# Kernel tuning notes

Measured on AMD Instinct MI355X. Metric: run time of the kernel, lower is better.

Reference implementation:

```python
import jax, jax.numpy as jnp
import numpy as np

N_VARS = 28
HID = 64
BATCH = 32768
BN_EPS = 1e-5


def _lin_init(key, fan_in, shape):
    bound = 1.0 / np.sqrt(fan_in)
    return jax.random.uniform(key, shape, minval=-bound, maxval=bound, dtype=jnp.float32)


def setup_inputs() -> dict:
    key = jax.random.key(0)
    ks = jax.random.split(key, 8)
    n, h = N_VARS, HID
    X = jax.random.normal(ks[0], (BATCH, n), dtype=jnp.float32)
    W_logits = jax.random.uniform(ks[1], (n, n), minval=-0.01, maxval=0.01, dtype=jnp.float32)
    # per-mechanism (grouped) weights, stacked on leading mechanism axis n
    W1 = _lin_init(ks[2], n, (n, h, n)); b1 = _lin_init(ks[3], n, (n, h))
    W2 = _lin_init(ks[4], h, (n, h, h)); b2 = _lin_init(ks[5], h, (n, h))
    W3 = _lin_init(ks[6], h, (n, 1, h)); b3 = _lin_init(ks[7], h, (n, 1))
    gamma1 = jnp.ones((n, h)); beta1 = jnp.zeros((n, h))
    gamma2 = jnp.ones((n, h)); beta2 = jnp.zeros((n, h))
    return {"X": X, "W_logits": W_logits,
            "W1": W1, "b1": b1, "gamma1": gamma1, "beta1": beta1,
            "W2": W2, "b2": b2, "gamma2": gamma2, "beta2": beta2,
            "W3": W3, "b3": b3}


def _bn(x, gamma, beta):
    # x: [n, B, h]; batch stats over B (training-mode BatchNorm1d, biased var)
    m = x.mean(axis=1, keepdims=True)
    v = ((x - m) ** 2).mean(axis=1, keepdims=True)
    return gamma[:, None, :] * (x - m) * jax.lax.rsqrt(v + BN_EPS) + beta[:, None, :]


def reference(X, W_logits, W1, b1, gamma1, beta1, W2, b2, gamma2, beta2, W3, b3):
    n = W_logits.shape[0]
    # adjacency: sigmoid with zeroed diagonal
    W = jax.nn.sigmoid(W_logits) * (1.0 - jnp.eye(n, dtype=W_logits.dtype))
    # fuse the parent mask into the first layer's weights: one grouped GEMM
    # instead of n_vars separate masked matmuls
    W1_eff = W1 * W[:, None, :]                               # [n, h, n]
    h1 = jnp.einsum('bd,nhd->nbh', X, W1_eff) + b1[:, None, :]  # [n, B, h]
    a1 = jax.nn.gelu(_bn(h1, gamma1, beta1), approximate=False)
    h2 = jnp.einsum('nbh,ngh->nbg', a1, W2) + b2[:, None, :]
    a2 = jax.nn.gelu(_bn(h2, gamma2, beta2), approximate=False)
    out = jnp.einsum('nbh,noh->nbo', a2, W3) + b3[:, None, :]   # [n, B, 1]
    X_hat = out[:, :, 0].T                                     # [B, n]
    return (X_hat, W)
```

## Files before the change

### kernel.cpp

```cpp
#include <hip/hip_runtime.h>
#include <hip/hip_bf16.h>
#include <math.h>

typedef float  f4 __attribute__((ext_vector_type(4)));
typedef short  s8 __attribute__((ext_vector_type(8)));
typedef short  s4 __attribute__((ext_vector_type(4)));
typedef int    i2 __attribute__((ext_vector_type(2)));

#define NV 28
#define NB 32768
#define BN_EPS 1e-5f
#define NSLOT 434

#define SUM2_OFF   0
#define SSQ2_OFF   1792
#define BIAS1_OFF  3584
#define GATE_OFF   5376
#define PART_OFF   9472
#define BF_BASE_F  120640
#define W2B_OFF_S  57344
#define XBF_OFF_S  172032
#define H2_BYTE_OFF 2924544ull
#define H2_BYTES    117440512ull

#define SMEM_BYTES 34816
#define GMAIN 896

__device__ __forceinline__ float gelu_f(float x) {
    float x2 = x * x;
    float z  = x * __builtin_fmaf(x2, -0.10294324f, -2.3022082f);
    float t  = __builtin_amdgcn_exp2f(z);
    return x * __builtin_amdgcn_rcpf(1.0f + t);
}
__device__ __forceinline__ unsigned short f2bf(float x) {
    unsigned u = __builtin_bit_cast(unsigned, x);
    return (unsigned short)((u + 0x7fffu + ((u >> 16) & 1u)) >> 16);
}
__device__ __forceinline__ int bfpack(float a, float b) {
    unsigned ua = __builtin_bit_cast(unsigned, a) + 0x8000u;
    unsigned ub = __builtin_bit_cast(unsigned, b) + 0x8000u;
    return __builtin_amdgcn_perm(ub, ua, 0x07060302);
}
__device__ __forceinline__ float row16_sum(float v) {
    int x;
    x = __builtin_amdgcn_update_dpp(0, __builtin_bit_cast(int, v), 0xB1, 0xF, 0xF, true);
    v += __builtin_bit_cast(float, x);
    x = __builtin_amdgcn_update_dpp(0, __builtin_bit_cast(int, v), 0x4E, 0xF, 0xF, true);
    v += __builtin_bit_cast(float, x);
    x = __builtin_amdgcn_update_dpp(0, __builtin_bit_cast(int, v), 0x124, 0xF, 0xF, true);
    v += __builtin_bit_cast(float, x);
    x = __builtin_amdgcn_update_dpp(0, __builtin_bit_cast(int, v), 0x128, 0xF, 0xF, true);
    v += __builtin_bit_cast(float, x);
    return v;
}
__device__ __forceinline__ float quad4_sum(float v) {
    int x;
    x = __builtin_amdgcn_update_dpp(0, __builtin_bit_cast(int, v), 0xB1, 0xF, 0xF, true);
    v += __builtin_bit_cast(float, x);
    x = __builtin_amdgcn_update_dpp(0, __builtin_bit_cast(int, v), 0x4E, 0xF, 0xF, true);
    v += __builtin_bit_cast(float, x);
    return v;
}

__global__ __launch_bounds__(256) void k_prep(const float* __restrict__ X,
                                              const float* __restrict__ Wlog,
                                              float* __restrict__ ws,
                                              float* __restrict__ out) {
    __shared__ float sx[128 * 28];
    const int b = blockIdx.x, tid = threadIdx.x;
    if (b == 256) {
        for (int i = tid; i < 3584; i += 256) ws[SUM2_OFF + i] = 0.0f;
        unsigned* gates = (unsigned*)(ws + GATE_OFF);
        for (int i = tid; i < 28 * 32; i += 256) gates[i] = 0u;
        for (int i = tid; i < 784; i += 256) {
            float w = 1.0f / (1.0f + expf(-Wlog[i]));
            if ((i / 28) == (i % 28)) w = 0.0f;
            out[917504 + i] = w;
        }
        return;
    }
    const int rowbase = b * 128;
    {
        const f4* src = (const f4*)(X + (size_t)rowbase * 28);
        f4* dst = (f4*)sx;
        for (int i = tid; i < 128 * 28 / 4; i += 256) dst[i] = src[i];
    }
    __syncthreads();
    int* xb = (int*)((short*)(ws + BF_BASE_F) + XBF_OFF_S);
    for (int j = tid; j < 128 * 16; j += 256) {
        int row = j >> 4, cc = j & 15;
        float lo = (2 * cc     < 28) ? sx[row * 28 + 2 * cc]     : 0.0f;
        float hi = (2 * cc + 1 < 28) ? sx[row * 28 + 2 * cc + 1] : 0.0f;
        xb[(size_t)(rowbase + row) * 16 + cc] = (int)f2bf(lo) | ((int)f2bf(hi) << 16);
    }
    for (int s = tid; s < NSLOT; s += 256) {
        float a = 0.0f;
        if (s < 28) {
            for (int r = 0; r < 128; ++r) a += sx[r * 28 + s];
        } else {
            int p = s - 28, d = 0, rem = 28;
            while (p >= rem) { p -= rem; ++d; --rem; }
            int e = d + p;
            for (int r = 0; r < 128; ++r)
                a = __builtin_fmaf(sx[r * 28 + d], sx[r * 28 + e], a);
        }
        ws[PART_OFF + b * NSLOT + s] = a;
    }
}

__global__ __launch_bounds__(256) void k_fold(const float* __restrict__ Wlog,
                                              const float* __restrict__ W1,
                                              const float* __restrict__ g1,
                                              const float* __restrict__ be1,
                                              const float* __restrict__ W2,
                                              float* __restrict__ ws) {
    __shared__ float sstat[NSLOT];
    __shared__ float mu[28], wrow[28];
    __shared__ float C[784];
    __shared__ float w1e_s[64 * 28];
    const int n = blockIdx.x, t = threadIdx.x;

    for (int s = t; s < NSLOT; s += 256) {
        float a = 0.0f;
#pragma unroll 16
        for (int p = 0; p < 256; ++p) a += ws[PART_OFF + p * NSLOT + s];
        sstat[s] = a;
    }
    __syncthreads();
    if (t < 28) {
        mu[t] = sstat[t] * (1.0f / 32768.0f);
        float w = 1.0f / (1.0f + expf(-Wlog[n * 28 + t]));
        if (t == n) w = 0.0f;
        wrow[t] = w;
    }
    __syncthreads();
    for (int i = t; i < 784; i += 256) {
        int d = i / 28, e = i % 28;
        int lo = d < e ? d : e, hi = d < e ? e : d;
        int idx = 28 + lo * 28 - (lo * (lo - 1)) / 2 + (hi - lo);
        C[i] = sstat[idx] * (1.0f / 32768.0f) - mu[d] * mu[e];
    }
    for (int i = t; i < 1792; i += 256)
        w1e_s[i] = W1[(size_t)n * 1792 + i] * wrow[i % 28];
    __syncthreads();

    const int h = t >> 2, j = t & 3;
    const float* we = &w1e_s[h * 28];
    float var_p = 0.0f, dot_p = 0.0f;
#pragma unroll
    for (int k = 0; k < 7; ++k) {
        int d = 7 * j + k;
        float inner = 0.0f;
#pragma unroll
        for (int e = 0; e < 28; ++e) inner = __builtin_fmaf(C[d * 28 + e], we[e], inner);
        float wd = we[d];
        var_p = __builtin_fmaf(inner, wd, var_p);
        dot_p = __builtin_fmaf(wd, mu[d], dot_p);
    }
    float var  = quad4_sum(var_p);
    float dotm = quad4_sum(dot_p);
    float scale = g1[n * 64 + h] * rsqrtf(fmaxf(var, 0.0f) + BN_EPS);
    if (j == 0)
        ws[BIAS1_OFF + n * 64 + h] = be1[n * 64 + h] - dotm * scale;

    short* bfbase = (short*)(ws + BF_BASE_F);
    {
        short* w1f = bfbase + (size_t)(n * 64 + h) * 32;
        s8 pk;
#pragma unroll
        for (int k = 0; k < 8; ++k) {
            int d = 8 * j + k;
            pk[k] = (short)f2bf(d < 28 ? we[d] * scale : 0.0f);
        }
        *(s8*)&w1f[8 * j] = pk;
    }
    {
        const float* w2src = W2 + (size_t)n * 4096 + t * 16;
        short* w2d = bfbase + W2B_OFF_S + (size_t)n * 4096 + t * 16;
        s8 a, b;
#pragma unroll
        for (int k = 0; k < 8; ++k) a[k] = (short)f2bf(w2src[k]);
#pragma unroll
        for (int k = 0; k < 8; ++k) b[k] = (short)f2bf(w2src[8 + k]);
        *(s8*)&w2d[0] = a;
        *(s8*)&w2d[8] = b;
    }
}

__device__ __forceinline__ void pass1_item(char* smemc, float* __restrict__ ws,
                                           short* __restrict__ h2buf, int item) {
    short* sW1 = (short*)smemc;
    short* sW2 = (short*)(smemc + 5120);
    short* sA1 = (short*)(smemc + 14336);
    float* sP1 = (float*)(smemc + 32768);
    float* sP2 = (float*)(smemc + 33792);
    const int n = item >> 7;
    const int blk = item & 127;
    const int tid = threadIdx.x;
    const int wave = tid >> 6;
    const int lane = tid & 63;
    const int m = lane & 15;
    const int q = lane >> 4;

    const short* bfbase = (const short*)(ws + BF_BASE_F);
    const short* w1g = bfbase + (size_t)n * 64 * 32;
    const short* w2g = bfbase + W2B_OFF_S + (size_t)n * 64 * 64;
    const short* xbf = bfbase + XBF_OFF_S;

    __syncthreads();
    {
        int r = tid >> 2, c = tid & 3;
        *(s8*)&sW1[r * 40 + c * 8] = *(const s8*)&w1g[r * 32 + c * 8];
#pragma unroll
        for (int k = 0; k < 2; ++k) {
            int i2x = tid + k * 256;
            int r2 = i2x >> 3, c2 = i2x & 7;
            *(s8*)&sW2[r2 * 72 + c2 * 8] = *(const s8*)&w2g[r2 * 64 + c2 * 8];
        }
    }
    __syncthreads();

    const float* bias1 = ws + BIAS1_OFF + n * 64;
    f4 biasv[4];
#pragma unroll
    for (int t = 0; t < 4; ++t) biasv[t] = *(const f4*)&bias1[16 * t + 4 * q];

    short* myA1a = &sA1[(wave * 2 + 0) * 16 * 72];
    short* myA1b = &sA1[(wave * 2 + 1) * 16 * 72];
    float s1[16], s2v[16];
#pragma unroll
    for (int i = 0; i < 16; ++i) { s1[i] = 0.0f; s2v[i] = 0.0f; }

#pragma unroll
    for (int it = 0; it < 2; ++it) {
        const int row0 = blk * 256 + it * 128 + wave * 32;
        s8 xfa = *(const s8*)&xbf[(size_t)(row0 + m) * 32 + 8 * q];
        s8 xfb = *(const s8*)&xbf[(size_t)(row0 + 16 + m) * 32 + 8 * q];

        f4 acc1a[4], acc1b[4];
#pragma unroll
        for (int t = 0; t < 4; ++t) {
            s8 wf = *(const s8*)&sW1[(16 * t + m) * 40 + q * 8];
            acc1a[t] = __builtin_amdgcn_mfma_f32_16x16x32_bf16(wf, xfa, (f4){0.f, 0.f, 0.f, 0.f}, 0, 0, 0);
            acc1b[t] = __builtin_amdgcn_mfma_f32_16x16x32_bf16(wf, xfb, (f4){0.f, 0.f, 0.f, 0.f}, 0, 0, 0);
        }
#pragma unroll
        for (int t = 0; t < 4; ++t) {
            float ga0 = gelu_f(acc1a[t][0] + biasv[t][0]);
            float ga1 = gelu_f(acc1a[t][1] + biasv[t][1]);
            float ga2 = gelu_f(acc1a[t][2] + biasv[t][2]);
            float ga3 = gelu_f(acc1a[t][3] + biasv[t][3]);
            float gb0 = gelu_f(acc1b[t][0] + biasv[t][0]);
            float gb1 = gelu_f(acc1b[t][1] + biasv[t][1]);
            float gb2 = gelu_f(acc1b[t][2] + biasv[t][2]);
            float gb3 = gelu_f(acc1b[t][3] + biasv[t][3]);
            i2 pa = (i2){bfpack(ga0, ga1), bfpack(ga2, ga3)};
            i2 pb = (i2){bfpack(gb0, gb1), bfpack(gb2, gb3)};
            *(i2*)&myA1a[m * 72 + 16 * t + 4 * q] = pa;
            *(i2*)&myA1b[m * 72 + 16 * t + 4 * q] = pb;
        }
        s8 af0a = *(const s8*)&myA1a[m * 72 + 8 * q];
        s8 af1a = *(const s8*)&myA1a[m * 72 + 32 + 8 * q];
        s8 af0b = *(const s8*)&myA1b[m * 72 + 8 * q];
        s8 af1b = *(const s8*)&myA1b[m * 72 + 32 + 8 * q];
        short* hpA = h2buf + ((size_t)n * NB + row0 + m) * 64;
        short* hpB = h2buf + ((size_t)n * NB + row0 + 16 + m) * 64;
#pragma unroll
        for (int u = 0; u < 4; ++u) {
            s8 w0 = *(const s8*)&sW2[(16 * u + m) * 72 + 8 * q];
            s8 w1 = *(const s8*)&sW2[(16 * u + m) * 72 + 32 + 8 * q];
            f4 aa = (f4){0.f, 0.f, 0.f, 0.f};
            f4 ab = (f4){0.f, 0.f, 0.f, 0.f};
            aa = __builtin_amdgcn_mfma_f32_16x16x32_bf16(w0, af0a, aa, 0, 0, 0);
            ab = __builtin_amdgcn_mfma_f32_16x16x32_bf16(w0, af0b, ab, 0, 0, 0);
            aa = __builtin_amdgcn_mfma_f32_16x16x32_bf16(w1, af1a, aa, 0, 0, 0);
            ab = __builtin_amdgcn_mfma_f32_16x16x32_bf16(w1, af1b, ab, 0, 0, 0);
            i2 ha = (i2){bfpack(aa[0], aa[1]), bfpack(aa[2], aa[3])};
            i2 hb = (i2){bfpack(ab[0], ab[1]), bfpack(ab[2], ab[3])};
            *(i2*)&hpA[16 * u + 4 * q] = ha;
            *(i2*)&hpB[16 * u + 4 * q] = hb;
#pragma unroll
            for (int r = 0; r < 4; ++r) {
                s1[u * 4 + r]  += aa[r] + ab[r];
                s2v[u * 4 + r] = __builtin_fmaf(aa[r], aa[r], s2v[u * 4 + r]);
                s2v[u * 4 + r] = __builtin_fmaf(ab[r], ab[r], s2v[u * 4 + r]);
            }
        }
    }
#pragma unroll
    for (int u = 0; u < 4; ++u) {
#pragma unroll
        for (int r = 0; r < 4; ++r) {
            float t1 = row16_sum(s1[u * 4 + r]);
            float t2 = row16_sum(s2v[u * 4 + r]);
            if (m == 0) {
                sP1[wave * 64 + 16 * u + 4 * q + r] = t1;
                sP2[wave * 64 + 16 * u + 4 * q + r] = t2;
            }
        }
    }
    __syncthreads();
    if (tid < 64) {
        float a = sP1[tid] + sP1[64 + tid] + sP1[128 + tid] + sP1[192 + tid];
        float b = sP2[tid] + sP2[64 + tid] + sP2[128 + tid] + sP2[192 + tid];
        atomicAdd(&ws[SUM2_OFF + n * 64 + tid], a);
        atomicAdd(&ws[SSQ2_OFF + n * 64 + tid], b);
    }
}

template <bool GATED>
__device__ __forceinline__ void pass2_item(char* smemc, const float* __restrict__ g2,
                                           const float* __restrict__ be2,
                                           const float* __restrict__ W3,
                                           const float* __restrict__ b3,
                                           float* __restrict__ ws,
                                           const short* __restrict__ h2buf,
                                           float* __restrict__ out, int item,
                                           unsigned* gates) {
    float* sSc  = (float*)smemc;
    float* sSh  = (float*)smemc + 64;
    float* sW3v = (float*)smemc + 128;
    const int n = item >> 7;
    const int rbase = (item & 127) * 256;
    const int tid = threadIdx.x;
    if (GATED && tid == 0) {
        while (__hip_atomic_load(&gates[n * 32], __ATOMIC_RELAXED, __HIP_MEMORY_SCOPE_AGENT) < 128u)
            __builtin_amdgcn_s_sleep(2);
    }
    __syncthreads();
    if (tid < 64) {
        float su, sq;
        if (GATED) {
            su = __hip_atomic_load(&ws[SUM2_OFF + n * 64 + tid], __ATOMIC_RELAXED, __HIP_MEMORY_SCOPE_AGENT);
            sq = __hip_atomic_load(&ws[SSQ2_OFF + n * 64 + tid], __ATOMIC_RELAXED, __HIP_MEMORY_SCOPE_AGENT);
        } else {
            su = ws[SUM2_OFF + n * 64 + tid];
            sq = ws[SSQ2_OFF + n * 64 + tid];
        }
        float mean = su * (1.0f / 32768.0f);
        float var  = sq * (1.0f / 32768.0f) - mean * mean;
        float sc = g2[n * 64 + tid] * rsqrtf(fmaxf(var, 0.0f) + BN_EPS);
        sSc[tid]  = sc;
        sSh[tid]  = be2[n * 64 + tid] - mean * sc;
        sW3v[tid] = W3[n * 64 + tid];
    }
    __syncthreads();
    const int wave = tid >> 6;
    const int lane = tid & 63;
    const int rr = lane >> 3;
    const int cc = lane & 7;
    f4 scA = *(const f4*)&sSc[cc * 8],  scB = *(const f4*)&sSc[cc * 8 + 4];
    f4 shA = *(const f4*)&sSh[cc * 8],  shB = *(const f4*)&sSh[cc * 8 + 4];
    f4 w3A = *(const f4*)&sW3v[cc * 8], w3B = *(const f4*)&sW3v[cc * 8 + 4];
    const float b3n = b3[n];
#pragma unroll
    for (int it = 0; it < 8; ++it) {
        const int row = rbase + wave * 64 + it * 8 + rr;
        s8 hv = *(const s8*)(h2buf + ((size_t)n * NB + row) * 64 + cc * 8);
        float p = 0.0f;
#pragma unroll
        for (int j = 0; j < 4; ++j) {
            float v = __builtin_fmaf(__builtin_bit_cast(float, ((int)(unsigned short)hv[j]) << 16), scA[j], shA[j]);
            p = __builtin_fmaf(gelu_f(v), w3A[j], p);
        }
#pragma unroll
        for (int j = 0; j < 4; ++j) {
            float v = __builtin_fmaf(__builtin_bit_cast(float, ((int)(unsigned short)hv[4 + j]) << 16), scB[j], shB[j]);
            p = __builtin_fmaf(gelu_f(v), w3B[j], p);
        }
        p += __shfl_xor(p, 1);
        p += __shfl_xor(p, 2);
        p += __shfl_xor(p, 4);
        if (cc == 0) out[(size_t)row * 28 + n] = p + b3n;
    }
}

__global__ __launch_bounds__(256, 4) void k_mainG(const float* __restrict__ g2,
                                                  const float* __restrict__ be2,
                                                  const float* __restrict__ W3,
                                                  const float* __restrict__ b3,
                                                  float* __restrict__ ws,
                                                  short* __restrict__ h2buf,
                                                  float* __restrict__ out) {
    __shared__ __align__(16) char smem[SMEM_BYTES];
    unsigned* gates = (unsigned*)(ws + GATE_OFF);
    const int b = blockIdx.x;
    const int tid = threadIdx.x;

#pragma unroll 1
    for (int k = 0; k < 4; ++k) {
        const int item = b + k * GMAIN;
        pass1_item(smem, ws, h2buf, item);
        __syncthreads();
        if (tid == 0)
            __hip_atomic_fetch_add(&gates[(item >> 7) * 32], 1u,
                                   __ATOMIC_RELAXED, __HIP_MEMORY_SCOPE_AGENT);
    }
#pragma unroll 1
    for (int k = 0; k < 4; ++k)
        pass2_item<true>(smem, g2, be2, W3, b3, ws, h2buf, out, b + k * GMAIN, gates);
}

__global__ __launch_bounds__(256, 4) void kf_p1(float* __restrict__ ws,
                                                short* __restrict__ h2buf) {
    __shared__ __align__(16) char smem[SMEM_BYTES];
    pass1_item(smem, ws, h2buf, blockIdx.x);
}
__global__ __launch_bounds__(256, 4) void kf_p2(const float* __restrict__ g2,
                                                const float* __restrict__ be2,
                                                const float* __restrict__ W3,
                                                const float* __restrict__ b3,
                                                float* __restrict__ ws,
                                                const short* __restrict__ h2buf,
                                                float* __restrict__ out) {
    __shared__ __align__(16) char smem[SMEM_BYTES];
    pass2_item<false>(smem, g2, be2, W3, b3, ws, h2buf, out, blockIdx.x, nullptr);
}

extern "C" void kernel_launch(void* const* d_in, const int* in_sizes, int n_in,
                              void* d_out, int out_size, void* d_ws, size_t ws_size,
                              hipStream_t stream) {
    const float* X   = (const float*)d_in[0];
    const float* Wl  = (const float*)d_in[1];
    const float* W1  = (const float*)d_in[2];
    const float* g1  = (const float*)d_in[4];
    const float* be1 = (const float*)d_in[5];
    const float* W2  = (const float*)d_in[6];
    const float* g2  = (const float*)d_in[8];
    const float* be2 = (const float*)d_in[9];
    const float* W3  = (const float*)d_in[10];
    const float* b3  = (const float*)d_in[11];
    float* out = (float*)d_out;
    float* ws  = (float*)d_ws;
    short* h2buf = (short*)((char*)d_ws + H2_BYTE_OFF);

    static int gmain = 0;
    if (gmain == 0) {
        int dev = 0;
        hipDeviceProp_t prop;
        bool ok = (hipGetDevice(&dev) == hipSuccess) &&
                  (hipGetDeviceProperties(&prop, dev) == hipSuccess) &&
                  prop.cooperativeLaunch;
        int bpc = 0;
        if (ok &&
            hipOccupancyMaxActiveBlocksPerMultiprocessor(&bpc, k_mainG, 256, 0) == hipSuccess &&
            (long)bpc * prop.multiProcessorCount >= GMAIN) {
            gmain = 1;
        } else {
            gmain = -1;
        }
    }

    k_prep<<<dim3(257), dim3(256), 0, stream>>>(X, Wl, ws, out);
    k_fold<<<dim3(28),  dim3(256), 0, stream>>>(Wl, W1, g1, be1, W2, ws);

    bool done = false;
    if (gmain > 0) {
        void* args[7] = {(void*)&g2, (void*)&be2, (void*)&W3, (void*)&b3,
                         (void*)&ws, (void*)&h2buf, (void*)&out};
        hipError_t e = hipLaunchCooperativeKernel(reinterpret_cast<const void*>(k_mainG),
                                                  dim3(GMAIN), dim3(256), args, 0, stream);
        if (e == hipSuccess) done = true;
        else gmain = -1;
    }
    if (!done) {
        kf_p1<<<dim3(3584), dim3(256), 0, stream>>>(ws, h2buf);
        kf_p2<<<dim3(3584), dim3(256), 0, stream>>>(g2, be2, W3, b3, ws, h2buf, out);
    }
}
```

Measured before the change: 177.8 us.

## Fuse weight folding into main kernel and shrink prep grid

```diff
diff --git a/kernel.cpp b/kernel.cpp
--- a/kernel.cpp
+++ b/kernel.cpp
@@ -4,27 +4,24 @@
 
 typedef float  f4 __attribute__((ext_vector_type(4)));
 typedef short  s8 __attribute__((ext_vector_type(8)));
-typedef short  s4 __attribute__((ext_vector_type(4)));
 typedef int    i2 __attribute__((ext_vector_type(2)));
 
 #define NV 28
 #define NB 32768
 #define BN_EPS 1e-5f
 #define NSLOT 434
+#define PBLK 32
 
 #define SUM2_OFF   0
 #define SSQ2_OFF   1792
-#define BIAS1_OFF  3584
 #define GATE_OFF   5376
 #define PART_OFF   9472
 #define BF_BASE_F  120640
-#define W2B_OFF_S  57344
 #define XBF_OFF_S  172032
 #define H2_BYTE_OFF 2924544ull
 #define H2_BYTES    117440512ull
 
-#define SMEM_BYTES 34816
-#define GMAIN 896
+#define SMEM_BYTES 35840
 
 __device__ __forceinline__ float gelu_f(float x) {
     float x2 = x * x;
@@ -60,6 +57,11 @@
     x = __builtin_amdgcn_update_dpp(0, __builtin_bit_cast(int, v), 0x4E, 0xF, 0xF, true);
     v += __builtin_bit_cast(float, x);
     return v;
+}
+__device__ __forceinline__ void slot_de(int s, int& d, int& e) {
+    int p = s - 28, dd = 0, rem = 28;
+    while (p >= rem) { p -= rem; ++dd; --rem; }
+    d = dd; e = dd + p;
 }
 
 __global__ __launch_bounds__(256) void k_prep(const float* __restrict__ X,
@@ -68,7 +70,7 @@
                                               float* __restrict__ out) {
     __shared__ float sx[128 * 28];
     const int b = blockIdx.x, tid = threadIdx.x;
-    if (b == 256) {
+    if (b == PBLK) {
         for (int i = tid; i < 3584; i += 256) ws[SUM2_OFF + i] = 0.0f;
         unsigned* gates = (unsigned*)(ws + GATE_OFF);
         for (int i = tid; i < 28 * 32; i += 256) gates[i] = 0u;
@@ -79,52 +81,80 @@
         }
         return;
     }
-    const int rowbase = b * 128;
-    {
-        const f4* src = (const f4*)(X + (size_t)rowbase * 28);
-        f4* dst = (f4*)sx;
-        for (int i = tid; i < 128 * 28 / 4; i += 256) dst[i] = src[i];
-    }
-    __syncthreads();
+    const int s0 = tid;
+    int d0 = 0, e0 = 0;
+    if (s0 >= 28) slot_de(s0, d0, e0);
+    const int s1 = tid + 256;
+    const bool h1v = (s1 < NSLOT);
+    int d1 = 0, e1 = 0;
+    if (h1v) slot_de(s1, d1, e1);
+
+    float a0 = 0.0f, a1 = 0.0f;
     int* xb = (int*)((short*)(ws + BF_BASE_F) + XBF_OFF_S);
-    for (int j = tid; j < 128 * 16; j += 256) {
-        int row = j >> 4, cc = j & 15;
-        float lo = (2 * cc     < 28) ? sx[row * 28 + 2 * cc]     : 0.0f;
-        float hi = (2 * cc + 1 < 28) ? sx[row * 28 + 2 * cc + 1] : 0.0f;
-        xb[(size_t)(rowbase + row) * 16 + cc] = (int)f2bf(lo) | ((int)f2bf(hi) << 16);
-    }
-    for (int s = tid; s < NSLOT; s += 256) {
-        float a = 0.0f;
-        if (s < 28) {
-            for (int r = 0; r < 128; ++r) a += sx[r * 28 + s];
+#pragma unroll 1
+    for (int ss = 0; ss < 8; ++ss) {
+        const int rowbase = b * 1024 + ss * 128;
+        __syncthreads();
+        {
+            const f4* src = (const f4*)(X + (size_t)rowbase * 28);
+            f4* dst = (f4*)sx;
+            for (int i = tid; i < 896; i += 256) dst[i] = src[i];
+        }
+        __syncthreads();
+        for (int j = tid; j < 2048; j += 256) {
+            int row = j >> 4, cc = j & 15;
+            float lo = (2 * cc     < 28) ? sx[row * 28 + 2 * cc]     : 0.0f;
+            float hi = (2 * cc + 1 < 28) ? sx[row * 28 + 2 * cc + 1] : 0.0f;
+            xb[(size_t)(rowbase + row) * 16 + cc] = (int)f2bf(lo) | ((int)f2bf(hi) << 16);
+        }
+        if (s0 < 28) {
+            for (int r = 0; r < 128; ++r) a0 += sx[r * 28 + s0];
         } else {
-            int p = s - 28, d = 0, rem = 28;
-            while (p >= rem) { p -= rem; ++d; --rem; }
-            int e = d + p;
             for (int r = 0; r < 128; ++r)
-                a = __builtin_fmaf(sx[r * 28 + d], sx[r * 28 + e], a);
-        }
-        ws[PART_OFF + b * NSLOT + s] = a;
-    }
-}
-
-__global__ __launch_bounds__(256) void k_fold(const float* __restrict__ Wlog,
-                                              const float* __restrict__ W1,
-                                              const float* __restrict__ g1,
-                                              const float* __restrict__ be1,
-                                              const float* __restrict__ W2,
-                                              float* __restrict__ ws) {
-    __shared__ float sstat[NSLOT];
-    __shared__ float mu[28], wrow[28];
-    __shared__ float C[784];
-    __shared__ float w1e_s[64 * 28];
-    const int n = blockIdx.x, t = threadIdx.x;
-
+                a0 = __builtin_fmaf(sx[r * 28 + d0], sx[r * 28 + e0], a0);
+        }
+        if (h1v) {
+            for (int r = 0; r < 128; ++r)
+                a1 = __builtin_fmaf(sx[r * 28 + d1], sx[r * 28 + e1], a1);
+        }
+    }
+    ws[PART_OFF + b * NSLOT + s0] = a0;
+    if (h1v) ws[PART_OFF + b * NSLOT + s1] = a1;
+}
+
+__device__ __forceinline__ void fold_local(char* smemc, const float* __restrict__ Wlog,
+                                           const float* __restrict__ W1,
+                                           const float* __restrict__ g1,
+                                           const float* __restrict__ be1,
+                                           const float* __restrict__ W2,
+                                           const float* __restrict__ ws, int n) {
+    short* sW1   = (short*)smemc;
+    short* sW2   = (short*)(smemc + 5120);
+    float* fb    = (float*)(smemc + 14336);
+    float* sstat = fb;
+    float* mu    = fb + 434;
+    float* wrow  = fb + 462;
+    float* C     = fb + 490;
+    float* w1e_s = fb + 1274;
+    float* sBias = (float*)(smemc + 34816);
+    const int t = threadIdx.x;
+
+    __syncthreads();
     for (int s = t; s < NSLOT; s += 256) {
         float a = 0.0f;
-#pragma unroll 16
-        for (int p = 0; p < 256; ++p) a += ws[PART_OFF + p * NSLOT + s];
+#pragma unroll 8
+        for (int p = 0; p < PBLK; ++p) a += ws[PART_OFF + p * NSLOT + s];
         sstat[s] = a;
+    }
+#pragma unroll
+    for (int k = 0; k < 2; ++k) {
+        int i = t + k * 256;
+        int r = i >> 3, c = i & 7;
+        const float* src = W2 + (size_t)n * 4096 + r * 64 + c * 8;
+        s8 pk;
+#pragma unroll
+        for (int j = 0; j < 8; ++j) pk[j] = (short)f2bf(src[j]);
+        *(s8*)&sW2[r * 72 + c * 8] = pk;
     }
     __syncthreads();
     if (t < 28) {
@@ -160,31 +190,17 @@
     float var  = quad4_sum(var_p);
     float dotm = quad4_sum(dot_p);
     float scale = g1[n * 64 + h] * rsqrtf(fmaxf(var, 0.0f) + BN_EPS);
-    if (j == 0)
-        ws[BIAS1_OFF + n * 64 + h] = be1[n * 64 + h] - dotm * scale;
-
-    short* bfbase = (short*)(ws + BF_BASE_F);
+    if (j == 0) sBias[h] = be1[n * 64 + h] - dotm * scale;
     {
-        short* w1f = bfbase + (size_t)(n * 64 + h) * 32;
         s8 pk;
 #pragma unroll
         for (int k = 0; k < 8; ++k) {
             int d = 8 * j + k;
             pk[k] = (short)f2bf(d < 28 ? we[d] * scale : 0.0f);
         }
-        *(s8*)&w1f[8 * j] = pk;
-    }
-    {
-        const float* w2src = W2 + (size_t)n * 4096 + t * 16;
-        short* w2d = bfbase + W2B_OFF_S + (size_t)n * 4096 + t * 16;
-        s8 a, b;
-#pragma unroll
-        for (int k = 0; k < 8; ++k) a[k] = (short)f2bf(w2src[k]);
-#pragma unroll
-        for (int k = 0; k < 8; ++k) b[k] = (short)f2bf(w2src[8 + k]);
-        *(s8*)&w2d[0] = a;
-        *(s8*)&w2d[8] = b;
-    }
+        *(s8*)&sW1[h * 40 + 8 * j] = pk;
+    }
+    __syncthreads();
 }
 
 __device__ __forceinline__ void pass1_item(char* smemc, float* __restrict__ ws,
@@ -194,6 +210,7 @@
     short* sA1 = (short*)(smemc + 14336);
     float* sP1 = (float*)(smemc + 32768);
     float* sP2 = (float*)(smemc + 33792);
+    float* sBias = (float*)(smemc + 34816);
     const int n = item >> 7;
     const int blk = item & 127;
     const int tid = threadIdx.x;
@@ -202,28 +219,12 @@
     const int m = lane & 15;
     const int q = lane >> 4;
 
-    const short* bfbase = (const short*)(ws + BF_BASE_F);
-    const short* w1g = bfbase + (size_t)n * 64 * 32;
-    const short* w2g = bfbase + W2B_OFF_S + (size_t)n * 64 * 64;
-    const short* xbf = bfbase + XBF_OFF_S;
-
-    __syncthreads();
-    {
-        int r = tid >> 2, c = tid & 3;
-        *(s8*)&sW1[r * 40 + c * 8] = *(const s8*)&w1g[r * 32 + c * 8];
-#pragma unroll
-        for (int k = 0; k < 2; ++k) {
-            int i2x = tid + k * 256;
-            int r2 = i2x >> 3, c2 = i2x & 7;
-            *(s8*)&sW2[r2 * 72 + c2 * 8] = *(const s8*)&w2g[r2 * 64 + c2 * 8];
-        }
-    }
-    __syncthreads();
-
-    const float* bias1 = ws + BIAS1_OFF + n * 64;
+    const short* xbf = (const short*)(ws + BF_BASE_F) + XBF_OFF_S;
+
+    __syncthreads();
     f4 biasv[4];
 #pragma unroll
-    for (int t = 0; t < 4; ++t) biasv[t] = *(const f4*)&bias1[16 * t + 4 * q];
+    for (int t = 0; t < 4; ++t) biasv[t] = *(const f4*)&sBias[16 * t + 4 * q];
 
     short* myA1a = &sA1[(wave * 2 + 0) * 16 * 72];
     short* myA1b = &sA1[(wave * 2 + 1) * 16 * 72];
@@ -317,9 +318,9 @@
                                            const short* __restrict__ h2buf,
                                            float* __restrict__ out, int item,
                                            unsigned* gates) {
-    float* sSc  = (float*)smemc;
-    float* sSh  = (float*)smemc + 64;
-    float* sW3v = (float*)smemc + 128;
+    float* sSc  = (float*)(smemc + 35072);
+    float* sSh  = (float*)(smemc + 35328);
+    float* sW3v = (float*)(smemc + 35584);
     const int n = item >> 7;
     const int rbase = (item & 127) * 256;
     const int tid = threadIdx.x;
@@ -375,7 +376,12 @@
     }
 }
 
-__global__ __launch_bounds__(256, 4) void k_mainG(const float* __restrict__ g2,
+__global__ __launch_bounds__(256, 4) void k_mainG(const float* __restrict__ Wlog,
+                                                  const float* __restrict__ W1,
+                                                  const float* __restrict__ g1,
+                                                  const float* __restrict__ be1,
+                                                  const float* __restrict__ W2,
+                                                  const float* __restrict__ g2,
                                                   const float* __restrict__ be2,
                                                   const float* __restrict__ W3,
                                                   const float* __restrict__ b3,
@@ -386,24 +392,39 @@
     unsigned* gates = (unsigned*)(ws + GATE_OFF);
     const int b = blockIdx.x;
     const int tid = threadIdx.x;
-
-#pragma unroll 1
-    for (int k = 0; k < 4; ++k) {
-        const int item = b + k * GMAIN;
-        pass1_item(smem, ws, h2buf, item);
-        __syncthreads();
-        if (tid == 0)
-            __hip_atomic_fetch_add(&gates[(item >> 7) * 32], 1u,
-                                   __ATOMIC_RELAXED, __HIP_MEMORY_SCOPE_AGENT);
-    }
-#pragma unroll 1
-    for (int k = 0; k < 4; ++k)
-        pass2_item<true>(smem, g2, be2, W3, b3, ws, h2buf, out, b + k * GMAIN, gates);
-}
-
-__global__ __launch_bounds__(256, 4) void kf_p1(float* __restrict__ ws,
+    const int I0 = 2 * b, I1 = 2 * b + 1, I2 = 2 * b + 1792, I3 = 2 * b + 1793;
+
+    fold_local(smem, Wlog, W1, g1, be1, W2, ws, I0 >> 7);
+    pass1_item(smem, ws, h2buf, I0);
+    __syncthreads();
+    if (tid == 0) __hip_atomic_fetch_add(&gates[(I0 >> 7) * 32], 1u, __ATOMIC_RELAXED, __HIP_MEMORY_SCOPE_AGENT);
+    pass1_item(smem, ws, h2buf, I1);
+    __syncthreads();
+    if (tid == 0) __hip_atomic_fetch_add(&gates[(I1 >> 7) * 32], 1u, __ATOMIC_RELAXED, __HIP_MEMORY_SCOPE_AGENT);
+
+    fold_local(smem, Wlog, W1, g1, be1, W2, ws, I2 >> 7);
+    pass1_item(smem, ws, h2buf, I2);
+    __syncthreads();
+    if (tid == 0) __hip_atomic_fetch_add(&gates[(I2 >> 7) * 32], 1u, __ATOMIC_RELAXED, __HIP_MEMORY_SCOPE_AGENT);
+    pass2_item<true>(smem, g2, be2, W3, b3, ws, h2buf, out, I0, gates);
+    pass1_item(smem, ws, h2buf, I3);
+    __syncthreads();
+    if (tid == 0) __hip_atomic_fetch_add(&gates[(I3 >> 7) * 32], 1u, __ATOMIC_RELAXED, __HIP_MEMORY_SCOPE_AGENT);
+
+    pass2_item<true>(smem, g2, be2, W3, b3, ws, h2buf, out, I1, gates);
+    pass2_item<true>(smem, g2, be2, W3, b3, ws, h2buf, out, I2, gates);
+    pass2_item<true>(smem, g2, be2, W3, b3, ws, h2buf, out, I3, gates);
+}
+
+__global__ __launch_bounds__(256, 4) void kf_p1(const float* __restrict__ Wlog,
+                                                const float* __restrict__ W1,
+                                                const float* __restrict__ g1,
+                                                const float* __restrict__ be1,
+                                                const float* __restrict__ W2,
+                                                float* __restrict__ ws,
                                                 short* __restrict__ h2buf) {
     __shared__ __align__(16) char smem[SMEM_BYTES];
+    fold_local(smem, Wlog, W1, g1, be1, W2, ws, (int)blockIdx.x >> 7);
     pass1_item(smem, ws, h2buf, blockIdx.x);
 }
 __global__ __launch_bounds__(256, 4) void kf_p2(const float* __restrict__ g2,
@@ -444,27 +465,27 @@
         int bpc = 0;
         if (ok &&
             hipOccupancyMaxActiveBlocksPerMultiprocessor(&bpc, k_mainG, 256, 0) == hipSuccess &&
-            (long)bpc * prop.multiProcessorCount >= GMAIN) {
+            (long)bpc * prop.multiProcessorCount >= 896) {
             gmain = 1;
         } else {
             gmain = -1;
         }
     }
 
-    k_prep<<<dim3(257), dim3(256), 0, stream>>>(X, Wl, ws, out);
-    k_fold<<<dim3(28),  dim3(256), 0, stream>>>(Wl, W1, g1, be1, W2, ws);
+    k_prep<<<dim3(PBLK + 1), dim3(256), 0, stream>>>(X, Wl, ws, out);
 
     bool done = false;
     if (gmain > 0) {
-        void* args[7] = {(void*)&g2, (void*)&be2, (void*)&W3, (void*)&b3,
-                         (void*)&ws, (void*)&h2buf, (void*)&out};
+        void* args[12] = {(void*)&Wl, (void*)&W1, (void*)&g1, (void*)&be1, (void*)&W2,
+                          (void*)&g2, (void*)&be2, (void*)&W3, (void*)&b3,
+                          (void*)&ws, (void*)&h2buf, (void*)&out};
         hipError_t e = hipLaunchCooperativeKernel(reinterpret_cast<const void*>(k_mainG),
-                                                  dim3(GMAIN), dim3(256), args, 0, stream);
+                                                  dim3(896), dim3(256), args, 0, stream);
         if (e == hipSuccess) done = true;
         else gmain = -1;
     }
     if (!done) {
-        kf_p1<<<dim3(3584), dim3(256), 0, stream>>>(ws, h2buf);
+        kf_p1<<<dim3(3584), dim3(256), 0, stream>>>(Wl, W1, g1, be1, W2, ws, h2buf);
         kf_p2<<<dim3(3584), dim3(256), 0, stream>>>(g2, be2, W3, b3, ws, h2buf, out);
     }
 }
```

After: 233.9 us. 1.32x slower.
